# Optimization experiments

Measured on AMD Instinct MI355X. Metric: run time of the kernel, lower is better.

## Reference

```python
import jax, jax.numpy as jnp
import numpy as np

D_MODEL = 1024
NUM_HEADS = 16
D_K = D_MODEL // NUM_HEADS


def setup_inputs() -> dict:
    key = jax.random.key(0)
    ks = jax.random.split(key, 11)
    B, S, D = 2, 2048, D_MODEL
    scale = 1.0 / np.sqrt(D)
    inp = {
        'q': jax.random.normal(ks[0], (B, S, D), jnp.float32),
        'k': jax.random.normal(ks[1], (B, S, D), jnp.float32),
        'v': jax.random.normal(ks[2], (B, S, D), jnp.float32),
        # torch nn.Linear weights are [out, in]; y = x @ W.T + b
        'Wq': jax.random.normal(ks[3], (D, D), jnp.float32) * scale,
        'bq': jax.random.normal(ks[4], (D,), jnp.float32) * scale,
        'Wk': jax.random.normal(ks[5], (D, D), jnp.float32) * scale,
        'bk': jax.random.normal(ks[6], (D,), jnp.float32) * scale,
        'Wv': jax.random.normal(ks[7], (D, D), jnp.float32) * scale,
        'bv': jax.random.normal(ks[8], (D,), jnp.float32) * scale,
        'Wo': jax.random.normal(ks[9], (D, D), jnp.float32) * scale,
        'bo': jax.random.normal(ks[10], (D,), jnp.float32) * scale,
    }
    return inp


def reference(q, k, v, Wq, bq, Wk, bk, Wv, bv, Wo, bo):
    B, S, D = q.shape
    H, dk = NUM_HEADS, D_K

    def proj(x, W, b):
        # torch Linear: x @ W.T + b ; then [B,S,H,dk] -> [B,H,S,dk]
        y = jnp.einsum('bsd,ed->bse', x, W) + b
        return y.reshape(B, S, H, dk).transpose(0, 2, 1, 3)

    Q = proj(q, Wq, bq)
    K = proj(k, Wk, bk)
    V = proj(v, Wv, bv)

    # NOTE: original module omits the 1/sqrt(d_k) scaling — faithful here.
    scores = jnp.einsum('bhqd,bhkd->bhqk', Q, K)  # [B,H,S,S]
    attn = jax.nn.softmax(scores, axis=-1)
    out = jnp.einsum('bhqk,bhkd->bhqd', attn, V)  # [B,H,S,dk]
    out = out.transpose(0, 2, 1, 3).reshape(B, S, D)
    return jnp.einsum('bsd,ed->bse', out, Wo) + bo
```

## Files before the change

### kernel.cpp

```cpp
#include <hip/hip_runtime.h>
#include <hip/hip_bf16.h>
#include <stdint.h>


using bf16 = __hip_bfloat16;
typedef __attribute__((ext_vector_type(8))) short v8s;
typedef __attribute__((ext_vector_type(4))) float v4f;

#define NB_ ((size_t)4194304)
#define ND_ ((size_t)1048576)

__device__ __forceinline__ void async16(const void* g, void* l) {
  __builtin_amdgcn_global_load_lds(
      (const __attribute__((address_space(1))) unsigned int*)g,
      (__attribute__((address_space(3))) unsigned int*)l, 16, 0, 0);
}

__device__ __forceinline__ v4f mfma16(v8s a, v8s b, v4f c) {
  return __builtin_amdgcn_mfma_f32_16x16x32_bf16(a, b, c, 0, 0, 0);
}

struct SplitArgs {
  const float4* src[7];
  ushort4* hi[7];
  ushort4* lo[7];
  int n4[7];
};

__global__ __launch_bounds__(256) void splitk(SplitArgs sa) {
  const int z = blockIdx.y;
  const float4* __restrict__ src = sa.src[z];
  ushort4* __restrict__ dh = sa.hi[z];
  ushort4* __restrict__ dl = sa.lo[z];
  const int n4 = sa.n4[z];
  const int stride = gridDim.x * blockDim.x;
  for (int i = blockIdx.x * blockDim.x + threadIdx.x; i < n4; i += stride) {
    const float4 x = src[i];
    float vals[4] = {x.x, x.y, x.z, x.w};
    unsigned short hs[4], ls[4];
#pragma unroll
    for (int j = 0; j < 4; ++j) {
      bf16 hb = __float2bfloat16(vals[j]);
      float rest = vals[j] - __bfloat162float(hb);
      bf16 lb = __float2bfloat16(rest);
      __builtin_memcpy(&hs[j], &hb, 2);
      __builtin_memcpy(&ls[j], &lb, 2);
    }
    ushort4 hv; hv.x = hs[0]; hv.y = hs[1]; hv.z = hs[2]; hv.w = hs[3];
    ushort4 lv; lv.x = ls[0]; lv.y = ls[1]; lv.z = ls[2]; lv.w = ls[3];
    dh[i] = hv;
    dl[i] = lv;
  }
}

struct GemmArgs {
  const bf16* Ah[3];
  const bf16* Al[3];
  const bf16* Bh[3];
  const bf16* Bl[3];
  const float* bias[3];
  void* O0[3];
  void* O1[3];
  int mode[3];
};

__global__ __launch_bounds__(256, 2) void gemm3t(GemmArgs ga) {
  const int z = blockIdx.z;
  const bf16* __restrict__ Ah = ga.Ah[z];
  const bf16* __restrict__ Al = ga.Al[z];
  const bf16* __restrict__ Bh = ga.Bh[z];
  const bf16* __restrict__ Bl = ga.Bl[z];
  const float* __restrict__ bias = ga.bias[z];
  const int mode = ga.mode[z];

  __shared__ alignas(16) bf16 lA0[128 * 32];
  __shared__ alignas(16) bf16 lA1[128 * 32];
  __shared__ alignas(16) bf16 lB0[128 * 32];
  __shared__ alignas(16) bf16 lB1[128 * 32];

  const int tid = threadIdx.x;
  const int lane = tid & 63;
  const int w = tid >> 6, wr = w >> 1, wc = w & 1;
  const int ln = lane & 15;
  const int h8 = (lane >> 4) * 8, h4 = (lane >> 4) * 4;
  const int m0 = blockIdx.y * 128, n0 = blockIdx.x * 128;

  v4f acc[4][4];
#pragma unroll
  for (int i = 0; i < 4; ++i)
#pragma unroll
    for (int j = 0; j < 4; ++j)
#pragma unroll
      for (int r = 0; r < 4; ++r) acc[i][j][r] = 0.f;

  for (int k0 = 0; k0 < 1024; k0 += 32) {
#pragma unroll
    for (int p = 0; p < 2; ++p) {
      const int idx = p * 256 + tid;
      const int row = idx >> 2, c8 = (idx & 3) * 8;
      const size_t gA = (size_t)(m0 + row) * 1024 + k0 + c8;
      const size_t gB = (size_t)(n0 + row) * 1024 + k0 + c8;
      async16(Ah + gA, &lA0[idx * 8]);
      async16(Al + gA, &lA1[idx * 8]);
      async16(Bh + gB, &lB0[idx * 8]);
      async16(Bl + gB, &lB1[idx * 8]);
    }
    __syncthreads();

    v8s a0[4], a1[4], b0[4], b1[4];
#pragma unroll
    for (int f = 0; f < 4; ++f) {
      const int ao = (wr * 64 + f * 16 + ln) * 32 + h8;
      const int bo = (wc * 64 + f * 16 + ln) * 32 + h8;
      a0[f] = *(const v8s*)&lA0[ao];
      a1[f] = *(const v8s*)&lA1[ao];
      b0[f] = *(const v8s*)&lB0[bo];
      b1[f] = *(const v8s*)&lB1[bo];
    }
#pragma unroll
    for (int i = 0; i < 4; ++i)
#pragma unroll
      for (int j = 0; j < 4; ++j) {
        acc[i][j] = mfma16(a0[i], b0[j], acc[i][j]);
        acc[i][j] = mfma16(a0[i], b1[j], acc[i][j]);
        acc[i][j] = mfma16(a1[i], b0[j], acc[i][j]);
      }
    __syncthreads();
  }

#pragma unroll
  for (int i = 0; i < 4; ++i)
#pragma unroll
    for (int j = 0; j < 4; ++j) {
      const int col = n0 + wc * 64 + j * 16 + ln;
      const float bb = bias[col];
#pragma unroll
      for (int r = 0; r < 4; ++r) {
        const int row = m0 + wr * 64 + i * 16 + h4 + r;
        const float vv = acc[i][j][r] + bb;
        if (mode == 2) {
          ((float*)ga.O0[z])[(size_t)row * 1024 + col] = vv;
        } else {
          const int b_ = row >> 11, s_ = row & 2047;
          const int hh = col >> 6, dd = col & 63;
          if (mode == 0) {
            const size_t o = (((size_t)(b_ * 16 + hh)) * 2048 + s_) * 64 + dd;
            bf16 hb = __float2bfloat16(vv);
            ((bf16*)ga.O0[z])[o] = hb;
            ((bf16*)ga.O1[z])[o] = __float2bfloat16(vv - __bfloat162float(hb));
          } else {
            const size_t o = (((size_t)(b_ * 16 + hh)) * 64 + dd) * 2048 + s_;
            ((bf16*)ga.O0[z])[o] = __float2bfloat16(vv);
          }
        }
      }
    }
}

__global__ __launch_bounds__(256, 2) void attnk(
    const bf16* __restrict__ Qh, const bf16* __restrict__ Ql,
    const bf16* __restrict__ Kh, const bf16* __restrict__ Kl,
    const bf16* __restrict__ Vt,
    bf16* __restrict__ Oh, bf16* __restrict__ Ol) {
  __shared__ alignas(16) bf16 lKh[2][64 * 64];
  __shared__ alignas(16) bf16 lKl[2][64 * 64];
  __shared__ alignas(16) bf16 lVt[2][64 * 64];
  __shared__ alignas(16) bf16 lP[4][32 * 72];

  const int tid = threadIdx.x;
  const int lane = tid & 63, w = tid >> 6;
  const int ln = lane & 15, g = lane >> 4;
  const int h8 = g * 8, h4 = g * 4;
  const int bh = blockIdx.y;
  const int q0 = blockIdx.x * 128 + w * 32;

  v8s qh[2][2], ql[2][2];
#pragma unroll
  for (int mf = 0; mf < 2; ++mf) {
    const size_t rowg = (size_t)bh * 2048 + q0 + mf * 16 + ln;
#pragma unroll
    for (int ks = 0; ks < 2; ++ks) {
      qh[mf][ks] = *(const v8s*)&Qh[rowg * 64 + ks * 32 + h8];
      ql[mf][ks] = *(const v8s*)&Ql[rowg * 64 + ks * 32 + h8];
    }
  }

  v4f O[2][4];
  float lpart[2][4];
#pragma unroll
  for (int mf = 0; mf < 2; ++mf) {
#pragma unroll
    for (int r = 0; r < 4; ++r) lpart[mf][r] = 0.f;
#pragma unroll
    for (int d = 0; d < 4; ++d)
#pragma unroll
      for (int r = 0; r < 4; ++r) O[mf][d][r] = 0.f;
  }

  auto stage = [&](int buf, int kv0) {
#pragma unroll
    for (int p = 0; p < 2; ++p) {
      const int idx = p * 256 + tid;
      const int row = idx >> 3;
      const int cs = ((idx & 7) ^ (row & 7)) * 8;
      const size_t gk = ((size_t)bh * 2048 + kv0 + row) * 64 + cs;
      async16(Kh + gk, &lKh[buf][idx * 8]);
      async16(Kl + gk, &lKl[buf][idx * 8]);
      const size_t gv = ((size_t)bh * 64 + row) * 2048 + kv0 + cs;
      async16(Vt + gv, &lVt[buf][idx * 8]);
    }
  };

  stage(0, 0);
  __syncthreads();

  for (int t = 0; t < 32; ++t) {
    const int cur = t & 1;
    if (t < 31) stage(cur ^ 1, (t + 1) * 64);

    v4f sacc[2][4];
#pragma unroll
    for (int mf = 0; mf < 2; ++mf)
#pragma unroll
      for (int kvf = 0; kvf < 4; ++kvf)
#pragma unroll
        for (int r = 0; r < 4; ++r) sacc[mf][kvf][r] = 0.f;

    const char* kbh = (const char*)&lKh[cur][0];
    const char* kbl = (const char*)&lKl[cur][0];
    const char* vbb = (const char*)&lVt[cur][0];

#pragma unroll
    for (int ks = 0; ks < 2; ++ks) {
      const int cbyte = (ks << 6) + (g << 4);
      v8s kh[4], kl[4];
#pragma unroll
      for (int kvf = 0; kvf < 4; ++kvf) {
        const int kr = kvf * 16 + ln;
        const int koff = (kr << 7) + (cbyte ^ ((kr & 7) << 4));
        kh[kvf] = *(const v8s*)(kbh + koff);
        kl[kvf] = *(const v8s*)(kbl + koff);
      }
      __builtin_amdgcn_s_setprio(1);
#pragma unroll
      for (int mf = 0; mf < 2; ++mf)
#pragma unroll
        for (int kvf = 0; kvf < 4; ++kvf) {
          sacc[mf][kvf] = mfma16(qh[mf][ks], kh[kvf], sacc[mf][kvf]);
          sacc[mf][kvf] = mfma16(qh[mf][ks], kl[kvf], sacc[mf][kvf]);
          sacc[mf][kvf] = mfma16(ql[mf][ks], kh[kvf], sacc[mf][kvf]);
        }
      __builtin_amdgcn_s_setprio(0);
    }

#pragma unroll
    for (int mf = 0; mf < 2; ++mf)
#pragma unroll
      for (int kvf = 0; kvf < 4; ++kvf)
#pragma unroll
        for (int r = 0; r < 4; ++r) {
          const float p = __expf(sacc[mf][kvf][r]);
          lpart[mf][r] += p;
          lP[w][(mf * 16 + h4 + r) * 72 + kvf * 16 + ln] = __float2bfloat16(p);
        }

#pragma unroll
    for (int ks = 0; ks < 2; ++ks) {
      const int cbyte = (ks << 6) + (g << 4);
      v8s pa[2], vb[4];
#pragma unroll
      for (int mf = 0; mf < 2; ++mf)
        pa[mf] = *(const v8s*)&lP[w][(mf * 16 + ln) * 72 + ks * 32 + h8];
#pragma unroll
      for (int dkf = 0; dkf < 4; ++dkf) {
        const int vr = dkf * 16 + ln;
        const int voff = (vr << 7) + (cbyte ^ ((vr & 7) << 4));
        vb[dkf] = *(const v8s*)(vbb + voff);
      }
      __builtin_amdgcn_s_setprio(1);
#pragma unroll
      for (int mf = 0; mf < 2; ++mf)
#pragma unroll
        for (int dkf = 0; dkf < 4; ++dkf)
          O[mf][dkf] = mfma16(pa[mf], vb[dkf], O[mf][dkf]);
      __builtin_amdgcn_s_setprio(0);
    }
    __syncthreads();
  }

  float lrow[2][4];
#pragma unroll
  for (int mf = 0; mf < 2; ++mf)
#pragma unroll
    for (int r = 0; r < 4; ++r) {
      float s = lpart[mf][r];
      s += __shfl_xor(s, 1, 64);
      s += __shfl_xor(s, 2, 64);
      s += __shfl_xor(s, 4, 64);
      s += __shfl_xor(s, 8, 64);
      lrow[mf][r] = s;
    }

  const int b_ = bh >> 4, hh = bh & 15;
#pragma unroll
  for (int mf = 0; mf < 2; ++mf)
#pragma unroll
    for (int r = 0; r < 4; ++r) {
      const float inv = 1.f / lrow[mf][r];
      const int s_ = blockIdx.x * 128 + w * 32 + mf * 16 + h4 + r;
#pragma unroll
      for (int dkf = 0; dkf < 4; ++dkf) {
        const float o = O[mf][dkf][r] * inv;
        const size_t off = ((size_t)b_ * 2048 + s_) * 1024 + hh * 64 + dkf * 16 + ln;
        bf16 hb = __float2bfloat16(o);
        Oh[off] = hb;
        Ol[off] = __float2bfloat16(o - __bfloat162float(hb));
      }
    }
}

extern "C" void kernel_launch(void* const* d_in, const int* in_sizes, int n_in,
                              void* d_out, int out_size, void* d_ws, size_t ws_size,
                              hipStream_t stream) {
  const float* q  = (const float*)d_in[0];
  const float* k  = (const float*)d_in[1];
  const float* v  = (const float*)d_in[2];
  const float* Wq = (const float*)d_in[3];
  const float* bq = (const float*)d_in[4];
  const float* Wk = (const float*)d_in[5];
  const float* bk = (const float*)d_in[6];
  const float* Wv = (const float*)d_in[7];
  const float* bv = (const float*)d_in[8];
  const float* Wo = (const float*)d_in[9];
  const float* bo = (const float*)d_in[10];

  const size_t NB = NB_, ND = ND_;
  bf16* P = (bf16*)d_ws;

  const bool fused = (ws_size >= (size_t)120 * 1024 * 1024);

  if (fused) {
    bf16 *qh = P, *ql = qh + NB, *kh = ql + NB, *kl = kh + NB, *vh = kl + NB, *vl = vh + NB;
    bf16 *wqh = vl + NB, *wql = wqh + ND, *wkh = wql + ND, *wkl = wkh + ND;
    bf16 *wvh = wkl + ND, *wvl = wvh + ND, *woh = wvl + ND, *wol = woh + ND;
    bf16 *Qh = wol + ND, *Ql = Qh + NB, *Kh2 = Ql + NB, *Kl2 = Kh2 + NB, *Vt = Kl2 + NB;
    bf16 *Ah = qh, *Al = ql;

    SplitArgs sa{};
    const float* srcs[7] = {q, k, v, Wq, Wk, Wv, Wo};
    bf16* his[7] = {qh, kh, vh, wqh, wkh, wvh, woh};
    bf16* los[7] = {ql, kl, vl, wql, wkl, wvl, wol};
    for (int i = 0; i < 7; ++i) {
      sa.src[i] = (const float4*)srcs[i];
      sa.hi[i] = (ushort4*)his[i];
      sa.lo[i] = (ushort4*)los[i];
      sa.n4[i] = (int)((i < 3 ? NB : ND) / 4);
    }
    splitk<<<dim3(512, 7), 256, 0, stream>>>(sa);

    GemmArgs ga{};
    ga.Ah[0] = qh; ga.Al[0] = ql; ga.Bh[0] = wqh; ga.Bl[0] = wql;
    ga.bias[0] = bq; ga.O0[0] = Qh; ga.O1[0] = Ql; ga.mode[0] = 0;
    ga.Ah[1] = kh; ga.Al[1] = kl; ga.Bh[1] = wkh; ga.Bl[1] = wkl;
    ga.bias[1] = bk; ga.O0[1] = Kh2; ga.O1[1] = Kl2; ga.mode[1] = 0;
    ga.Ah[2] = vh; ga.Al[2] = vl; ga.Bh[2] = wvh; ga.Bl[2] = wvl;
    ga.bias[2] = bv; ga.O0[2] = Vt; ga.O1[2] = nullptr; ga.mode[2] = 1;
    gemm3t<<<dim3(8, 32, 3), 256, 0, stream>>>(ga);

    attnk<<<dim3(16, 32), 256, 0, stream>>>(Qh, Ql, Kh2, Kl2, Vt, Ah, Al);

    GemmArgs go{};
    go.Ah[0] = Ah; go.Al[0] = Al; go.Bh[0] = woh; go.Bl[0] = wol;
    go.bias[0] = bo; go.O0[0] = d_out; go.O1[0] = nullptr; go.mode[0] = 2;
    gemm3t<<<dim3(8, 32, 1), 256, 0, stream>>>(go);
  } else {
    bf16 *ash = P, *asl = ash + NB, *wsh = asl + NB, *wsl = wsh + ND;
    bf16 *Qh = wsl + ND, *Ql = Qh + NB, *Kh2 = Ql + NB, *Kl2 = Kh2 + NB, *Vt = Kl2 + NB;

    auto do_split2 = [&](const float* a, const float* wsrc) {
      SplitArgs s{};
      s.src[0] = (const float4*)a; s.hi[0] = (ushort4*)ash; s.lo[0] = (ushort4*)asl;
      s.n4[0] = (int)(NB / 4);
      s.src[1] = (const float4*)wsrc; s.hi[1] = (ushort4*)wsh; s.lo[1] = (ushort4*)wsl;
      s.n4[1] = (int)(ND / 4);
      splitk<<<dim3(512, 2), 256, 0, stream>>>(s);
    };
    auto do_gemm = [&](const float* bias, void* o0, void* o1, int mode) {
      GemmArgs g{};
      g.Ah[0] = ash; g.Al[0] = asl; g.Bh[0] = wsh; g.Bl[0] = wsl;
      g.bias[0] = bias; g.O0[0] = o0; g.O1[0] = o1; g.mode[0] = mode;
      gemm3t<<<dim3(8, 32, 1), 256, 0, stream>>>(g);
    };

    do_split2(q, Wq); do_gemm(bq, Qh, Ql, 0);
    do_split2(k, Wk); do_gemm(bk, Kh2, Kl2, 0);
    do_split2(v, Wv); do_gemm(bv, Vt, nullptr, 1);

    attnk<<<dim3(16, 32), 256, 0, stream>>>(Qh, Ql, Kh2, Kl2, Vt, ash, asl);

    SplitArgs s4{};
    s4.src[0] = (const float4*)Wo; s4.hi[0] = (ushort4*)wsh; s4.lo[0] = (ushort4*)wsl;
    s4.n4[0] = (int)(ND / 4);
    splitk<<<dim3(512, 1), 256, 0, stream>>>(s4);
    GemmArgs g4{};
    g4.Ah[0] = ash; g4.Al[0] = asl; g4.Bh[0] = wsh; g4.Bl[0] = wsl;
    g4.bias[0] = bo; g4.O0[0] = d_out; g4.O1[0] = nullptr; g4.mode[0] = 2;
    gemm3t<<<dim3(8, 32, 1), 256, 0, stream>>>(g4);
  }
}
```

Before: 333.7 us.

## Swizzle GEMM LDS layout, template M-tile, use 64-row tiles for output projection

The projection GEMM gets an XOR swizzle on the 16-byte column chunks in LDS so that fragment reads avoid bank conflicts. The kernel is templated on the M tile size: the QKV GEMM keeps 128-row tiles with occupancy raised to 3 blocks per SM, and the output projection uses 64-row tiles to launch twice as many blocks. Wave priority is raised around the MFMA block to favour compute issue. Smaller tiles for the output GEMM trade operand reuse for better CU fill, and the higher occupancy bound may pressure registers.

New measurement: 325.0 us. 2.6% less time.

```diff
diff --git a/kernel.cpp b/kernel.cpp
--- a/kernel.cpp
+++ b/kernel.cpp
@@ -64,7 +64,9 @@
   int mode[3];
 };
 
-__global__ __launch_bounds__(256, 2) void gemm3t(GemmArgs ga) {
+template <int TM>
+__global__ __launch_bounds__(256, TM == 128 ? 3 : 2) void gemm3t(GemmArgs ga) {
+  constexpr int MFR = TM / 32;
   const int z = blockIdx.z;
   const bf16* __restrict__ Ah = ga.Ah[z];
   const bf16* __restrict__ Al = ga.Al[z];
@@ -73,70 +75,89 @@
   const float* __restrict__ bias = ga.bias[z];
   const int mode = ga.mode[z];
 
-  __shared__ alignas(16) bf16 lA0[128 * 32];
-  __shared__ alignas(16) bf16 lA1[128 * 32];
+  __shared__ alignas(16) bf16 lA0[TM * 32];
+  __shared__ alignas(16) bf16 lA1[TM * 32];
   __shared__ alignas(16) bf16 lB0[128 * 32];
   __shared__ alignas(16) bf16 lB1[128 * 32];
 
   const int tid = threadIdx.x;
   const int lane = tid & 63;
   const int w = tid >> 6, wr = w >> 1, wc = w & 1;
-  const int ln = lane & 15;
-  const int h8 = (lane >> 4) * 8, h4 = (lane >> 4) * 4;
-  const int m0 = blockIdx.y * 128, n0 = blockIdx.x * 128;
-
-  v4f acc[4][4];
-#pragma unroll
-  for (int i = 0; i < 4; ++i)
+  const int ln = lane & 15, g = lane >> 4;
+  const int h4 = g * 4;
+  const int m0 = blockIdx.y * TM, n0 = blockIdx.x * 128;
+
+  v4f acc[MFR][4];
+#pragma unroll
+  for (int i = 0; i < MFR; ++i)
 #pragma unroll
     for (int j = 0; j < 4; ++j)
 #pragma unroll
       for (int r = 0; r < 4; ++r) acc[i][j][r] = 0.f;
 
   for (int k0 = 0; k0 < 1024; k0 += 32) {
+#pragma unroll
+    for (int p = 0; p < TM / 64; ++p) {
+      const int idx = p * 256 + tid;
+      const int row = idx >> 2, c = idx & 3;
+      const int cs = (c ^ (row & 3)) * 8;
+      const size_t gA = (size_t)(m0 + row) * 1024 + k0 + cs;
+      async16(Ah + gA, &lA0[idx * 8]);
+      async16(Al + gA, &lA1[idx * 8]);
+    }
 #pragma unroll
     for (int p = 0; p < 2; ++p) {
       const int idx = p * 256 + tid;
-      const int row = idx >> 2, c8 = (idx & 3) * 8;
-      const size_t gA = (size_t)(m0 + row) * 1024 + k0 + c8;
-      const size_t gB = (size_t)(n0 + row) * 1024 + k0 + c8;
-      async16(Ah + gA, &lA0[idx * 8]);
-      async16(Al + gA, &lA1[idx * 8]);
+      const int row = idx >> 2, c = idx & 3;
+      const int cs = (c ^ (row & 3)) * 8;
+      const size_t gB = (size_t)(n0 + row) * 1024 + k0 + cs;
       async16(Bh + gB, &lB0[idx * 8]);
       async16(Bl + gB, &lB1[idx * 8]);
     }
     __syncthreads();
 
-    v8s a0[4], a1[4], b0[4], b1[4];
+    const char* pA0 = (const char*)lA0;
+    const char* pA1 = (const char*)lA1;
+    const char* pB0 = (const char*)lB0;
+    const char* pB1 = (const char*)lB1;
+
+    v8s a0[MFR], a1[MFR], b0[4], b1[4];
+#pragma unroll
+    for (int f = 0; f < MFR; ++f) {
+      const int row = wr * (TM / 2) + f * 16 + ln;
+      const int off = (row << 6) + ((g ^ (row & 3)) << 4);
+      a0[f] = *(const v8s*)(pA0 + off);
+      a1[f] = *(const v8s*)(pA1 + off);
+    }
 #pragma unroll
     for (int f = 0; f < 4; ++f) {
-      const int ao = (wr * 64 + f * 16 + ln) * 32 + h8;
-      const int bo = (wc * 64 + f * 16 + ln) * 32 + h8;
-      a0[f] = *(const v8s*)&lA0[ao];
-      a1[f] = *(const v8s*)&lA1[ao];
-      b0[f] = *(const v8s*)&lB0[bo];
-      b1[f] = *(const v8s*)&lB1[bo];
-    }
-#pragma unroll
-    for (int i = 0; i < 4; ++i)
+      const int row = wc * 64 + f * 16 + ln;
+      const int off = (row << 6) + ((g ^ (row & 3)) << 4);
+      b0[f] = *(const v8s*)(pB0 + off);
+      b1[f] = *(const v8s*)(pB1 + off);
+    }
+    __builtin_amdgcn_s_setprio(1);
+#pragma unroll
+    for (int i = 0; i < MFR; ++i)
 #pragma unroll
       for (int j = 0; j < 4; ++j) {
         acc[i][j] = mfma16(a0[i], b0[j], acc[i][j]);
         acc[i][j] = mfma16(a0[i], b1[j], acc[i][j]);
         acc[i][j] = mfma16(a1[i], b0[j], acc[i][j]);
       }
+    __builtin_amdgcn_s_setprio(0);
     __syncthreads();
   }
 
 #pragma unroll
-  for (int i = 0; i < 4; ++i)
+  for (int i = 0; i < MFR; ++i)
 #pragma unroll
     for (int j = 0; j < 4; ++j) {
       const int col = n0 + wc * 64 + j * 16 + ln;
       const float bb = bias[col];
 #pragma unroll
       for (int r = 0; r < 4; ++r) {
-        const int row = m0 + wr * 64 + i * 16 + h4 + r;
+        const int row = m0 + wr * (TM / 2) + i * 16 + h4 + r;
         const float vv = acc[i][j][r] + bb;
         if (mode == 2) {
           ((float*)ga.O0[z])[(size_t)row * 1024 + col] = vv;
@@ -365,14 +386,14 @@
     ga.bias[1] = bk; ga.O0[1] = Kh2; ga.O1[1] = Kl2; ga.mode[1] = 0;
     ga.Ah[2] = vh; ga.Al[2] = vl; ga.Bh[2] = wvh; ga.Bl[2] = wvl;
     ga.bias[2] = bv; ga.O0[2] = Vt; ga.O1[2] = nullptr; ga.mode[2] = 1;
-    gemm3t<<<dim3(8, 32, 3), 256, 0, stream>>>(ga);
+    gemm3t<128><<<dim3(8, 32, 3), 256, 0, stream>>>(ga);
 
     attnk<<<dim3(16, 32), 256, 0, stream>>>(Qh, Ql, Kh2, Kl2, Vt, Ah, Al);
 
     GemmArgs go{};
     go.Ah[0] = Ah; go.Al[0] = Al; go.Bh[0] = woh; go.Bl[0] = wol;
     go.bias[0] = bo; go.O0[0] = d_out; go.O1[0] = nullptr; go.mode[0] = 2;
-    gemm3t<<<dim3(8, 32, 1), 256, 0, stream>>>(go);
+    gemm3t<64><<<dim3(8, 64, 1), 256, 0, stream>>>(go);
   } else {
     bf16 *ash = P, *asl = ash + NB, *wsh = asl + NB, *wsl = wsh + ND;
     bf16 *Qh = wsl + ND, *Ql = Qh + NB, *Kh2 = Ql + NB, *Kl2 = Kh2 + NB, *Vt = Kl2 + NB;
@@ -389,7 +410,7 @@
       GemmArgs g{};
       g.Ah[0] = ash; g.Al[0] = asl; g.Bh[0] = wsh; g.Bl[0] = wsl;
       g.bias[0] = bias; g.O0[0] = o0; g.O1[0] = o1; g.mode[0] = mode;
-      gemm3t<<<dim3(8, 32, 1), 256, 0, stream>>>(g);
+      gemm3t<128><<<dim3(8, 32, 1), 256, 0, stream>>>(g);
     };
 
     do_split2(q, Wq); do_gemm(bq, Qh, Ql, 0);
@@ -405,6 +426,6 @@
     GemmArgs g4{};
     g4.Ah[0] = ash; g4.Al[0] = asl; g4.Bh[0] = wsh; g4.Bl[0] = wsl;
     g4.bias[0] = bo; g4.O0[0] = d_out; g4.O1[0] = nullptr; g4.mode[0] = 2;
-    gemm3t<<<dim3(8, 32, 1), 256, 0, stream>>>(g4);
-  }
-}
+    gemm3t<64><<<dim3(8, 64, 1), 256, 0, stream>>>(g4);
+  }
+}
```
